# Kernel optimization log

Measured on AMD Instinct MI355X. Metric: run time of the kernel, lower is better.

## Reference

```python
import jax, jax.numpy as jnp
import numpy as np

N_NODES = 100000
N_EDGES = 1600000
N_REL = 8
IN_CH = 64
HIDDEN = 64
OUT_CH = 32


def setup_inputs() -> dict:
    key = jax.random.key(0)
    ks = jax.random.split(key, 10)
    s_in = 1.0 / np.sqrt(IN_CH)
    s_h = 1.0 / np.sqrt(HIDDEN)
    return {
        "x": jax.random.normal(ks[0], (N_NODES, IN_CH), dtype=jnp.float32),
        "edge_index": jax.random.randint(ks[1], (2, N_EDGES), 0, N_NODES, dtype=jnp.int64),
        "edge_type": jax.random.randint(ks[2], (N_EDGES,), 0, N_REL, dtype=jnp.int64),
        "W0": jax.random.normal(ks[3], (N_REL, IN_CH, HIDDEN), dtype=jnp.float32) * s_in,
        "Q0": jax.random.normal(ks[4], (HIDDEN, 1), dtype=jnp.float32) * s_h,
        "K0": jax.random.normal(ks[5], (HIDDEN, 1), dtype=jnp.float32) * s_h,
        "b0": jnp.zeros((HIDDEN,), dtype=jnp.float32),
        "W1": jax.random.normal(ks[6], (N_REL, HIDDEN, OUT_CH), dtype=jnp.float32) * s_h,
        "Q1": jax.random.normal(ks[7], (OUT_CH, 1), dtype=jnp.float32) * (1.0 / np.sqrt(OUT_CH)),
        "K1": jax.random.normal(ks[8], (OUT_CH, 1), dtype=jnp.float32) * (1.0 / np.sqrt(OUT_CH)),
        "b1": jnp.zeros((OUT_CH,), dtype=jnp.float32),
    }


def rgat_conv(x, src, dst, et, W, Q, K, b, n_nodes):
    # relation-typed transform of all nodes: [R, N, out]
    xw = jnp.einsum("ni,rio->rno", x, W)
    # per-node, per-relation attention logits (heads=1, dim=1)
    q = jnp.einsum("rno,od->rnd", xw, Q)[..., 0]  # [R, N]
    k = jnp.einsum("rno,od->rnd", xw, K)[..., 0]  # [R, N]
    # additive self-attention, leaky_relu slope 0.2 (PyG RGATConv default)
    alpha = jax.nn.leaky_relu(q[et, dst] + k[et, src], negative_slope=0.2)  # [E]
    # across-relation segment softmax over incoming edges of each dst node
    amax = jax.ops.segment_max(alpha, dst, num_segments=n_nodes)
    a = jnp.exp(alpha - amax[dst])
    denom = jax.ops.segment_sum(a, dst, num_segments=n_nodes)
    a = a / (denom[dst] + 1e-16)
    # weighted scatter-add aggregation of transformed source features
    msg = a[:, None] * xw[et, src]  # [E, out]
    return jax.ops.segment_sum(msg, dst, num_segments=n_nodes) + b


def reference(x, edge_index, edge_type, W0, Q0, K0, b0, W1, Q1, K1, b1):
    src, dst = edge_index[0], edge_index[1]
    n = x.shape[0]
    h = rgat_conv(x, src, dst, edge_type, W0, Q0, K0, b0, n)
    h = jax.nn.relu(h)  # dropout p=0.0 -> identity
    out = rgat_conv(h, src, dst, edge_type, W1, Q1, K1, b1, n)
    return out
```

## Files before the change

### kernel.cpp

```cpp
#include <hip/hip_runtime.h>
#include <hip/hip_bf16.h>
#include <math.h>


#define CSR_CHUNK 8192

__global__ void k_bhist(const int* __restrict__ dst, int* __restrict__ bcount,
                        int E, int NB) {
    __shared__ int h[512];
    int t = threadIdx.x;
    for (int i = t; i < NB; i += 256) h[i] = 0;
    __syncthreads();
    int e0 = blockIdx.x * CSR_CHUNK;
    int e1 = min(e0 + CSR_CHUNK, E);
    for (int i = e0 + t; i < e1; i += 256) atomicAdd(&h[dst[i] >> 8], 1);
    __syncthreads();
    for (int i = t; i < NB; i += 256) {
        int c = h[i];
        if (c) atomicAdd(&bcount[i], c);
    }
}

__global__ void k_bscan(const int* __restrict__ bcount, int* __restrict__ bstart,
                        int* __restrict__ gcur, int* __restrict__ rowptr,
                        int NB, int N, int E) {
    __shared__ int s[512];
    int t = threadIdx.x;
    int v = (t < NB) ? bcount[t] : 0;
    s[t] = v;
    __syncthreads();
    for (int off = 1; off < 512; off <<= 1) {
        int a = (t >= off) ? s[t - off] : 0;
        __syncthreads();
        s[t] += a;
        __syncthreads();
    }
    int excl = s[t] - v;
    if (t < NB) {
        bstart[t] = excl;
        gcur[t] = excl;
    }
    if (t == 0) {
        bstart[NB] = E;
        rowptr[N] = E;
    }
}

__global__ void k_bscatter(const int* __restrict__ src, const int* __restrict__ dst,
                           const int* __restrict__ et, int* __restrict__ gcur,
                           unsigned* __restrict__ ebuf, int E, int NB) {
    __shared__ int h[512];
    __shared__ int basearr[512];
    int t = threadIdx.x;
    for (int i = t; i < NB; i += 256) h[i] = 0;
    __syncthreads();
    int e0 = blockIdx.x * CSR_CHUNK;
    int e1 = min(e0 + CSR_CHUNK, E);
    for (int i = e0 + t; i < e1; i += 256) atomicAdd(&h[dst[i] >> 8], 1);
    __syncthreads();
    for (int i = t; i < NB; i += 256) {
        int c = h[i];
        basearr[i] = c ? atomicAdd(&gcur[i], c) : 0;
        h[i] = 0;
    }
    __syncthreads();
    for (int i = e0 + t; i < e1; i += 256) {
        int d = dst[i];
        int b = d >> 8;
        int off = atomicAdd(&h[b], 1);
        ebuf[basearr[b] + off] =
            ((unsigned)(d & 255) << 20) | ((unsigned)et[i] << 17) | (unsigned)src[i];
    }
}

__global__ void k_bsort(const unsigned* __restrict__ ebuf, const int* __restrict__ bstart,
                        int* __restrict__ rowptr, int* __restrict__ csr, int N) {
    __shared__ int lh[2048];
    __shared__ int ls[2048];
    __shared__ int ss[256];
    int b = blockIdx.x, t = threadIdx.x;
    int e0 = bstart[b], e1 = bstart[b + 1];
    for (int i = t; i < 2048; i += 256) lh[i] = 0;
    __syncthreads();
    for (int i = e0 + t; i < e1; i += 256) {
        unsigned u = ebuf[i];
        atomicAdd(&lh[(int)(((u >> 20) & 255) * 8 + ((u >> 17) & 7))], 1);
    }
    __syncthreads();
    int loc[8];
    int s = 0;
#pragma unroll
    for (int j = 0; j < 8; j++) {
        loc[j] = s;
        s += lh[t * 8 + j];
    }
    ss[t] = s;
    __syncthreads();
    for (int off = 1; off < 256; off <<= 1) {
        int a = (t >= off) ? ss[t - off] : 0;
        __syncthreads();
        ss[t] += a;
        __syncthreads();
    }
    int excl = ss[t] - s;
#pragma unroll
    for (int j = 0; j < 8; j++) ls[t * 8 + j] = excl + loc[j];
    int node = b * 256 + t;
    if (node < N) rowptr[node] = e0 + excl;
    __syncthreads();
    for (int i = t; i < 2048; i += 256) lh[i] = 0;
    __syncthreads();
    for (int i = e0 + t; i < e1; i += 256) {
        unsigned u = ebuf[i];
        int key = (int)(((u >> 20) & 255) * 8 + ((u >> 17) & 7));
        int off = atomicAdd(&lh[key], 1);
        csr[e0 + ls[key] + off] = (int)(u & 0xFFFFF);
    }
}


__global__ void k_wt2(const float* __restrict__ W, __hip_bfloat16* __restrict__ hi,
                      __hip_bfloat16* __restrict__ lo, int OUT, int total) {
    int t = blockIdx.x * blockDim.x + threadIdx.x;
    if (t < total) {
        int per = 64 * OUT;
        int r = t / per;
        int rem = t % per;
        int i = rem / OUT;
        int o = rem % OUT;
        float v = W[t];
        __hip_bfloat16 h = __float2bfloat16(v);
        __hip_bfloat16 l = __float2bfloat16(v - __bfloat162float(h));
        size_t idx = (size_t)o * 512 + i * 8 + r;
        hi[idx] = h;
        lo[idx] = l;
    }
}

__global__ void k_wqk(const float* W, const float* Qv, const float* Kv,
                      float* wq, float* wk, int OUT) {
    int t = blockIdx.x * blockDim.x + threadIdx.x;
    if (t < 8 * 64) {
        int r = t >> 6, i = t & 63;
        const float* wrow = W + ((size_t)r * 64 + i) * OUT;
        float a = 0.f, b = 0.f;
        for (int o = 0; o < OUT; o++) {
            float w = wrow[o];
            a += w * Qv[o];
            b += w * Kv[o];
        }
        wq[t] = a;
        wk[t] = b;
    }
}

__global__ __launch_bounds__(256) void k_qk2(
        const float* __restrict__ xin, const float* __restrict__ wq,
        const float* __restrict__ wk, float* __restrict__ qn,
        float* __restrict__ kn, unsigned short* __restrict__ xbb, int N) {
    __shared__ float xt[64][65];
    __shared__ float swq[8 * 65], swk[8 * 65];
    int t = threadIdx.x;
    int nb0 = blockIdx.x * 64;
    for (int i = t; i < 512; i += 256) {
        int r = i >> 6, c = i & 63;
        swq[r * 65 + c] = wq[i];
        swk[r * 65 + c] = wk[i];
    }
    for (int i = t; i < 1024; i += 256) {
        int ns = i >> 4;
        int c4 = i & 15;
        int n = nb0 + ns;
        float4 v = {0.f, 0.f, 0.f, 0.f};
        if (n < N) v = ((const float4*)xin)[(size_t)n * 16 + c4];
        xt[ns][c4 * 4 + 0] = v.x;
        xt[ns][c4 * 4 + 1] = v.y;
        xt[ns][c4 * 4 + 2] = v.z;
        xt[ns][c4 * 4 + 3] = v.w;
        if (n < N) {
            __hip_bfloat16 b0 = __float2bfloat16(v.x);
            __hip_bfloat16 b1 = __float2bfloat16(v.y);
            __hip_bfloat16 b2 = __float2bfloat16(v.z);
            __hip_bfloat16 b3 = __float2bfloat16(v.w);
            ushort4 o;
            o.x = *(unsigned short*)&b0;
            o.y = *(unsigned short*)&b1;
            o.z = *(unsigned short*)&b2;
            o.w = *(unsigned short*)&b3;
            *(ushort4*)(xbb + (size_t)n * 64 + c4 * 4) = o;
        }
    }
    __syncthreads();
#pragma unroll
    for (int g = t; g < 512; g += 256) {
        int ns = g >> 3, r = g & 7;
        int n = nb0 + ns;
        if (n < N) {
            float qa = 0.f, ka = 0.f;
#pragma unroll
            for (int i = 0; i < 64; i++) {
                float xv = xt[ns][i];
                qa += xv * swq[r * 65 + i];
                ka += xv * swk[r * 65 + i];
            }
            qn[(size_t)n * 8 + r] = qa;
            kn[(size_t)n * 8 + r] = ka;
        }
    }
}

#define ZSTR 520
#define EMAX 512

#define FLUSH8()                          \
    do {                                  \
        switch (currel) {                 \
            case 0: a0 += racc; break;    \
            case 1: a1 += racc; break;    \
            case 2: a2 += racc; break;    \
            case 3: a3 += racc; break;    \
            case 4: a4 += racc; break;    \
            case 5: a5 += racc; break;    \
            case 6: a6 += racc; break;    \
            case 7: a7 += racc; break;    \
        }                                 \
    } while (0)

template <int OUT, bool RELU>
__global__ __launch_bounds__(256) void k_fused(
        const int* __restrict__ rowptr, const int* __restrict__ csr,
        const float* __restrict__ qn, const float* __restrict__ kn,
        const unsigned short* __restrict__ xb,
        const __hip_bfloat16* __restrict__ wthi,
        const __hip_bfloat16* __restrict__ wtlo,
        const float* __restrict__ bias, float* __restrict__ xout, int N) {
    using v8s = __attribute__((ext_vector_type(8))) short;
    using v4f = __attribute__((ext_vector_type(4))) float;
    __shared__ unsigned short zt[16 * ZSTR];
    __shared__ uint2 s_rec[EMAX];
    __shared__ int s_rp[17];
    __shared__ float s_q[128];
    __shared__ float s_den[16];
    int t = threadIdx.x;
    int wv = t >> 6;
    int lane = t & 63;
    int nb0 = blockIdx.x * 16;

    if (t < 17) {
        int nd = nb0 + t;
        s_rp[t] = rowptr[nd > N ? N : nd];
    }
    if (t < 128) {
        int nd = nb0 + (t >> 3);
        s_q[t] = (nd < N) ? qn[(size_t)nd * 8 + (t & 7)] : 0.f;
    }
    if (t < 16) s_den[t] = 0.f;
    __syncthreads();
    int e0 = s_rp[0];
    int esz = s_rp[16] - e0;

    if (esz <= EMAX) {
        for (int i = t; i < esz; i += 256) {
            int ge = e0 + i;
            int pk = csr[ge];
            int lo = 0;
            lo = (s_rp[lo + 8] <= ge) ? lo + 8 : lo;
            lo = (s_rp[lo + 4] <= ge) ? lo + 4 : lo;
            lo = (s_rp[lo + 2] <= ge) ? lo + 2 : lo;
            lo = (s_rp[lo + 1] <= ge) ? lo + 1 : lo;
            int rel = pk >> 17;
            int src = pk & 0x1FFFF;
            float v = s_q[lo * 8 + rel] + kn[(size_t)src * 8 + rel];
            v = (v >= 0.f) ? v : 0.2f * v;
            float tv = __expf(v);
            atomicAdd(&s_den[lo], tv);
            s_rec[i] = uint2{__float_as_uint(tv), (unsigned)pk};
        }
        __syncthreads();

#pragma unroll 1
        for (int q = 0; q < 4; q++) {
            int nl = wv * 4 + q;
            int r0 = s_rp[nl] - e0;
            int r1 = s_rp[nl + 1] - e0;
            float a0 = 0.f, a1 = 0.f, a2 = 0.f, a3 = 0.f;
            float a4 = 0.f, a5 = 0.f, a6 = 0.f, a7 = 0.f;
            int currel = 0;
            float racc = 0.f;
#pragma unroll 1
            for (int j = r0; j < r1; j += 16) {
                float tvv[16];
                int pkk[16];
#pragma unroll
                for (int u = 0; u < 16; u++) {
                    int ii = j + u;
                    bool ok = ii < r1;
                    ii = ok ? ii : (r1 - 1);
                    uint2 rc = s_rec[ii];
                    tvv[u] = __uint_as_float(
                        __builtin_amdgcn_readfirstlane((int)(ok ? rc.x : 0u)));
                    pkk[u] = __builtin_amdgcn_readfirstlane((int)rc.y);
                }
                unsigned short xu[16];
#pragma unroll
                for (int u = 0; u < 16; u++)
                    xu[u] = xb[(size_t)(pkk[u] & 0x1FFFF) * 64 + lane];
#pragma unroll
                for (int u = 0; u < 16; u++) {
                    int rl = pkk[u] >> 17;
                    if (rl != currel) {
                        FLUSH8();
                        currel = rl;
                        racc = 0.f;
                    }
                    racc += tvv[u] * __uint_as_float(((unsigned)xu[u]) << 16);
                }
            }
            FLUSH8();
            float inv = 1.f / (s_den[nl] + 1e-16f);
            float av[8] = {a0, a1, a2, a3, a4, a5, a6, a7};
            unsigned short us[8];
#pragma unroll
            for (int r = 0; r < 8; r++) {
                __hip_bfloat16 b = __float2bfloat16(av[r] * inv);
                us[r] = *(unsigned short*)&b;
            }
            uint4 pack;
            pack.x = (unsigned)us[0] | ((unsigned)us[1] << 16);
            pack.y = (unsigned)us[2] | ((unsigned)us[3] << 16);
            pack.z = (unsigned)us[4] | ((unsigned)us[5] << 16);
            pack.w = (unsigned)us[6] | ((unsigned)us[7] << 16);
            *(uint4*)&zt[nl * ZSTR + lane * 8] = pack;
        }
    } else {
        for (int q = 0; q < 4; q++) {
            int nl = wv * 4 + q;
            int wid = nb0 + nl;
            uint4 pack = {0u, 0u, 0u, 0u};
            if (wid < N) {
                int r0 = rowptr[wid], r1 = rowptr[wid + 1];
                float qv = (lane < 8) ? qn[wid * 8 + lane] : 0.f;
                float denom = 0.f;
                float a0 = 0.f, a1 = 0.f, a2 = 0.f, a3 = 0.f;
                float a4 = 0.f, a5 = 0.f, a6 = 0.f, a7 = 0.f;
                int currel = 0;
                float racc = 0.f;

                for (int base = r0; base < r1; base += 64) {
                    int s = base + lane;
                    int pk = (s < r1) ? csr[s] : 0;
                    int src = pk & 0x1FFFF;
                    int rel = pk >> 17;
                    float qq = __shfl(qv, rel, 64);
                    float tv = 0.f;
                    if (s < r1) {
                        float v = qq + kn[src * 8 + rel];
                        v = (v >= 0.f) ? v : 0.2f * v;
                        tv = __expf(v);
                    }
                    float ts = tv;
#pragma unroll
                    for (int off = 32; off > 0; off >>= 1) ts += __shfl_xor(ts, off, 64);
                    denom += ts;

                    int cnt = min(64, r1 - base);
                    int tvi = (int)__float_as_uint(tv);
                    for (int j = 0; j < cnt; j += 16) {
                        unsigned p[16];
                        float tf[16];
#pragma unroll
                        for (int u = 0; u < 16; u++) {
                            p[u] = (unsigned)__builtin_amdgcn_readlane(pk, j + u);
                            tf[u] = __uint_as_float(
                                (unsigned)__builtin_amdgcn_readlane(tvi, j + u));
                        }
                        unsigned xg[16];
#pragma unroll
                        for (int u = 0; u < 16; u++)
                            xg[u] = (unsigned)xb[(size_t)(p[u] & 0x1FFFF) * 64 + lane];
#pragma unroll
                        for (int u = 0; u < 16; u++) {
                            int rl = (int)(p[u] >> 17);
                            if (rl != currel) {
                                FLUSH8();
                                currel = rl;
                                racc = 0.f;
                            }
                            racc += tf[u] * __uint_as_float(xg[u] << 16);
                        }
                    }
                }
                FLUSH8();
                float inv = 1.f / (denom + 1e-16f);
                float av[8] = {a0, a1, a2, a3, a4, a5, a6, a7};
                unsigned short us[8];
#pragma unroll
                for (int r = 0; r < 8; r++) {
                    __hip_bfloat16 b = __float2bfloat16(av[r] * inv);
                    us[r] = *(unsigned short*)&b;
                }
                pack.x = (unsigned)us[0] | ((unsigned)us[1] << 16);
                pack.y = (unsigned)us[2] | ((unsigned)us[3] << 16);
                pack.z = (unsigned)us[4] | ((unsigned)us[5] << 16);
                pack.w = (unsigned)us[6] | ((unsigned)us[7] << 16);
            }
            *(uint4*)&zt[nl * ZSTR + lane * 8] = pack;
        }
    }
    __syncthreads();

    int quad = lane >> 4;
    int l15 = lane & 15;
    int nt = wv;
    if (nt * 16 < OUT) {
        const short* wh = (const short*)wthi;
        const short* wl = (const short*)wtlo;
        v4f acc = {0.f, 0.f, 0.f, 0.f};
#pragma unroll
        for (int k0 = 0; k0 < 512; k0 += 32) {
            int koff = k0 + quad * 8;
            v8s A = *(const v8s*)&zt[l15 * ZSTR + koff];
            v8s bh = *(const v8s*)(wh + (size_t)(nt * 16 + l15) * 512 + koff);
            v8s bl = *(const v8s*)(wl + (size_t)(nt * 16 + l15) * 512 + koff);
            acc = __builtin_amdgcn_mfma_f32_16x16x32_bf16(A, bh, acc, 0, 0, 0);
            acc = __builtin_amdgcn_mfma_f32_16x16x32_bf16(A, bl, acc, 0, 0, 0);
        }
        float bcol = bias[nt * 16 + l15];
#pragma unroll
        for (int g = 0; g < 4; g++) {
            int row = nb0 + quad * 4 + g;
            if (row < N) {
                float o = acc[g] + bcol;
                if (RELU) o = fmaxf(o, 0.f);
                xout[(size_t)row * OUT + nt * 16 + l15] = o;
            }
        }
    }
}


extern "C" void kernel_launch(void* const* d_in, const int* in_sizes, int n_in,
                              void* d_out, int out_size, void* d_ws, size_t ws_size,
                              hipStream_t stream) {
    const float* x   = (const float*)d_in[0];
    const int*   ei  = (const int*)d_in[1];
    const int*   et  = (const int*)d_in[2];
    const float* W0  = (const float*)d_in[3];
    const float* Q0  = (const float*)d_in[4];
    const float* K0  = (const float*)d_in[5];
    const float* b0  = (const float*)d_in[6];
    const float* W1  = (const float*)d_in[7];
    const float* Q1  = (const float*)d_in[8];
    const float* K1  = (const float*)d_in[9];
    const float* b1  = (const float*)d_in[10];
    float* out = (float*)d_out;

    const int N = in_sizes[0] / 64;
    const int E = in_sizes[2];
    const int* src = ei;
    const int* dst = ei + E;
    const int NB = (N + 255) >> 8;

    char* p = (char*)d_ws;
    auto alloc = [&](size_t bytes) -> void* {
        void* r = (void*)p;
        p += ((bytes + 255) / 256) * 256;
        return r;
    };
    int* rowptr   = (int*)alloc((size_t)(N + 1) * 4);
    int* bcount   = (int*)alloc(513 * 4);
    int* bstart   = (int*)alloc(513 * 4);
    int* gcur     = (int*)alloc(513 * 4);
    unsigned* ebuf = (unsigned*)alloc((size_t)E * 4);
    int* csr      = (int*)alloc((size_t)E * 4);
    float* wq     = (float*)alloc(8 * 64 * 4);
    float* wk     = (float*)alloc(8 * 64 * 4);
    float* qn     = (float*)alloc((size_t)N * 8 * 4);
    float* kn     = (float*)alloc((size_t)N * 8 * 4);
    __hip_bfloat16* wthi = (__hip_bfloat16*)alloc((size_t)64 * 512 * 2);
    __hip_bfloat16* wtlo = (__hip_bfloat16*)alloc((size_t)64 * 512 * 2);
    float* h      = (float*)alloc((size_t)N * 64 * 4);
    unsigned short* xbb = (unsigned short*)alloc((size_t)N * 64 * 2);

    int nchunks = (E + CSR_CHUNK - 1) / CSR_CHUNK;
    hipMemsetAsync(bcount, 0, (size_t)NB * 4, stream);
    k_bhist<<<nchunks, 256, 0, stream>>>(dst, bcount, E, NB);
    k_bscan<<<1, 512, 0, stream>>>(bcount, bstart, gcur, rowptr, NB, N, E);
    k_bscatter<<<nchunks, 256, 0, stream>>>(src, dst, et, gcur, ebuf, E, NB);
    k_bsort<<<NB, 256, 0, stream>>>(ebuf, bstart, rowptr, csr, N);

    int nfb = (N + 15) / 16;
    int nqkb = (N + 63) / 64;

    k_wqk<<<2, 256, 0, stream>>>(W0, Q0, K0, wq, wk, 64);
    k_qk2<<<nqkb, 256, 0, stream>>>(x, wq, wk, qn, kn, xbb, N);
    k_wt2<<<(8 * 64 * 64 + 255) / 256, 256, 0, stream>>>(W0, wthi, wtlo, 64, 8 * 64 * 64);
    k_fused<64, true><<<nfb, 256, 0, stream>>>(rowptr, csr, qn, kn, xbb,
                                               wthi, wtlo, b0, h, N);

    k_wqk<<<2, 256, 0, stream>>>(W1, Q1, K1, wq, wk, 32);
    k_qk2<<<nqkb, 256, 0, stream>>>(h, wq, wk, qn, kn, xbb, N);
    k_wt2<<<(8 * 64 * 32 + 255) / 256, 256, 0, stream>>>(W1, wthi, wtlo, 32, 8 * 64 * 32);
    k_fused<32, false><<<nfb, 256, 0, stream>>>(rowptr, csr, qn, kn, xbb,
                                                wthi, wtlo, b1, out, N);
}
```

Measured before the change: 438.3 us.

## Double-buffer edge gathers across a wave's four nodes with node id packed in CSR

```diff
diff --git a/kernel.cpp b/kernel.cpp
--- a/kernel.cpp
+++ b/kernel.cpp
@@ -114,7 +114,7 @@
         unsigned u = ebuf[i];
         int key = (int)(((u >> 20) & 255) * 8 + ((u >> 17) & 7));
         int off = atomicAdd(&lh[key], 1);
-        csr[e0 + ls[key] + off] = (int)(u & 0xFFFFF);
+        csr[e0 + ls[key] + off] = (int)u;
     }
 }
 
@@ -226,6 +226,65 @@
         }                                 \
     } while (0)
 
+#define WRITEZ()                                                         \
+    do {                                                                 \
+        if (curnode >= 0) {                                              \
+            float inv = 1.f / (denom + 1e-16f);                          \
+            float av[8] = {a0, a1, a2, a3, a4, a5, a6, a7};              \
+            unsigned short us8[8];                                       \
+            _Pragma("unroll") for (int r = 0; r < 8; r++) {              \
+                __hip_bfloat16 bb = __float2bfloat16(av[r] * inv);       \
+                us8[r] = *(unsigned short*)&bb;                          \
+            }                                                            \
+            uint4 pk4;                                                   \
+            pk4.x = (unsigned)us8[0] | ((unsigned)us8[1] << 16);         \
+            pk4.y = (unsigned)us8[2] | ((unsigned)us8[3] << 16);         \
+            pk4.z = (unsigned)us8[4] | ((unsigned)us8[5] << 16);         \
+            pk4.w = (unsigned)us8[6] | ((unsigned)us8[7] << 16);         \
+            *(uint4*)&zt[curnode * ZSTR + lane * 8] = pk4;               \
+        }                                                                \
+    } while (0)
+
+#define LOADREC(PK, TV, g)                                               \
+    do {                                                                 \
+        int base_ = er0 + (g) * 16;                                      \
+        _Pragma("unroll") for (int u = 0; u < 16; u++) {                 \
+            int ii_ = base_ + u;                                         \
+            bool ok_ = ii_ < er1;                                        \
+            int ic_ = ok_ ? ii_ : (er1 - 1);                             \
+            uint2 rc_ = s_rec[ic_];                                      \
+            TV[u] = __uint_as_float(                                     \
+                __builtin_amdgcn_readfirstlane((int)(ok_ ? rc_.x : 0u)));\
+            PK[u] = __builtin_amdgcn_readfirstlane((int)rc_.y);          \
+        }                                                                \
+    } while (0)
+
+#define ISSUE(PK, XU)                                                    \
+    _Pragma("unroll") for (int u = 0; u < 16; u++)                       \
+        XU[u] = xb[(size_t)(PK[u] & 0x1FFFF) * 64 + lane];
+
+#define DRAIN(PK, TV, XU)                                                \
+    _Pragma("unroll") for (int u = 0; u < 16; u++) {                     \
+        int pk_ = PK[u];                                                 \
+        int nl_ = (pk_ >> 20) & 15;                                      \
+        int rl_ = (pk_ >> 17) & 7;                                       \
+        if (nl_ != curnode) {                                            \
+            FLUSH8();                                                    \
+            WRITEZ();                                                    \
+            curnode = nl_;                                               \
+            currel = rl_;                                                \
+            racc = 0.f;                                                  \
+            denom = 0.f;                                                 \
+            a0 = a1 = a2 = a3 = a4 = a5 = a6 = a7 = 0.f;                 \
+        } else if (rl_ != currel) {                                      \
+            FLUSH8();                                                    \
+            currel = rl_;                                                \
+            racc = 0.f;                                                  \
+        }                                                                \
+        racc += TV[u] * __uint_as_float(((unsigned)XU[u]) << 16);        \
+        denom += TV[u];                                                  \
+    }
+
 template <int OUT, bool RELU>
 __global__ __launch_bounds__(256) void k_fused(
         const int* __restrict__ rowptr, const int* __restrict__ csr,
@@ -240,7 +299,6 @@
     __shared__ uint2 s_rec[EMAX];
     __shared__ int s_rp[17];
     __shared__ float s_q[128];
-    __shared__ float s_den[16];
     int t = threadIdx.x;
     int wv = t >> 6;
     int lane = t & 63;
@@ -254,83 +312,67 @@
         int nd = nb0 + (t >> 3);
         s_q[t] = (nd < N) ? qn[(size_t)nd * 8 + (t & 7)] : 0.f;
     }
-    if (t < 16) s_den[t] = 0.f;
+    {
+        uint4 zz = {0u, 0u, 0u, 0u};
+#pragma unroll
+        for (int q = 0; q < 4; q++)
+            *(uint4*)&zt[(wv * 4 + q) * ZSTR + lane * 8] = zz;
+    }
     __syncthreads();
     int e0 = s_rp[0];
     int esz = s_rp[16] - e0;
 
     if (esz <= EMAX) {
         for (int i = t; i < esz; i += 256) {
-            int ge = e0 + i;
-            int pk = csr[ge];
-            int lo = 0;
-            lo = (s_rp[lo + 8] <= ge) ? lo + 8 : lo;
-            lo = (s_rp[lo + 4] <= ge) ? lo + 4 : lo;
-            lo = (s_rp[lo + 2] <= ge) ? lo + 2 : lo;
-            lo = (s_rp[lo + 1] <= ge) ? lo + 1 : lo;
-            int rel = pk >> 17;
+            int pk = csr[e0 + i];
+            int nl = (pk >> 20) & 15;
+            int rel = (pk >> 17) & 7;
             int src = pk & 0x1FFFF;
-            float v = s_q[lo * 8 + rel] + kn[(size_t)src * 8 + rel];
+            float v = s_q[nl * 8 + rel] + kn[(size_t)src * 8 + rel];
             v = (v >= 0.f) ? v : 0.2f * v;
             float tv = __expf(v);
-            atomicAdd(&s_den[lo], tv);
             s_rec[i] = uint2{__float_as_uint(tv), (unsigned)pk};
         }
         __syncthreads();
 
-#pragma unroll 1
-        for (int q = 0; q < 4; q++) {
-            int nl = wv * 4 + q;
-            int r0 = s_rp[nl] - e0;
-            int r1 = s_rp[nl + 1] - e0;
+        {
+            int er0 = __builtin_amdgcn_readfirstlane(s_rp[wv * 4] - e0);
+            int er1 = __builtin_amdgcn_readfirstlane(s_rp[wv * 4 + 4] - e0);
+            int nG = (er1 - er0 + 15) >> 4;
+            int pkA[16], pkB[16];
+            float tvA[16], tvB[16];
+            unsigned short xuA[16], xuB[16];
             float a0 = 0.f, a1 = 0.f, a2 = 0.f, a3 = 0.f;
             float a4 = 0.f, a5 = 0.f, a6 = 0.f, a7 = 0.f;
-            int currel = 0;
-            float racc = 0.f;
+            float racc = 0.f, denom = 0.f;
+            int currel = 0, curnode = -1;
+
+            if (nG > 0) {
+                LOADREC(pkA, tvA, 0);
+                ISSUE(pkA, xuA);
+                bool curA = true;
 #pragma unroll 1
-            for (int j = r0; j < r1; j += 16) {
-                float tvv[16];
-                int pkk[16];
-#pragma unroll
-                for (int u = 0; u < 16; u++) {
-                    int ii = j + u;
-                    bool ok = ii < r1;
-                    ii = ok ? ii : (r1 - 1);
-                    uint2 rc = s_rec[ii];
-                    tvv[u] = __uint_as_float(
-                        __builtin_amdgcn_readfirstlane((int)(ok ? rc.x : 0u)));
-                    pkk[u] = __builtin_amdgcn_readfirstlane((int)rc.y);
+                for (int g = 0; g < nG; g++) {
+                    if (g + 1 < nG) {
+                        if (curA) {
+                            LOADREC(pkB, tvB, g + 1);
+                            ISSUE(pkB, xuB);
+                        } else {
+                            LOADREC(pkA, tvA, g + 1);
+                            ISSUE(pkA, xuA);
+                        }
+                    }
+                    __builtin_amdgcn_sched_barrier(0);
+                    if (curA) {
+                        DRAIN(pkA, tvA, xuA);
+                    } else {
+                        DRAIN(pkB, tvB, xuB);
+                    }
+                    curA = !curA;
                 }
-                unsigned short xu[16];
-#pragma unroll
-                for (int u = 0; u < 16; u++)
-                    xu[u] = xb[(size_t)(pkk[u] & 0x1FFFF) * 64 + lane];
-#pragma unroll
-                for (int u = 0; u < 16; u++) {
-                    int rl = pkk[u] >> 17;
-                    if (rl != currel) {
-                        FLUSH8();
-                        currel = rl;
-                        racc = 0.f;
-                    }
-                    racc += tvv[u] * __uint_as_float(((unsigned)xu[u]) << 16);
-                }
+                FLUSH8();
+                WRITEZ();
             }
-            FLUSH8();
-            float inv = 1.f / (s_den[nl] + 1e-16f);
-            float av[8] = {a0, a1, a2, a3, a4, a5, a6, a7};
-            unsigned short us[8];
-#pragma unroll
-            for (int r = 0; r < 8; r++) {
-                __hip_bfloat16 b = __float2bfloat16(av[r] * inv);
-                us[r] = *(unsigned short*)&b;
-            }
-            uint4 pack;
-            pack.x = (unsigned)us[0] | ((unsigned)us[1] << 16);
-            pack.y = (unsigned)us[2] | ((unsigned)us[3] << 16);
-            pack.z = (unsigned)us[4] | ((unsigned)us[5] << 16);
-            pack.w = (unsigned)us[6] | ((unsigned)us[7] << 16);
-            *(uint4*)&zt[nl * ZSTR + lane * 8] = pack;
         }
     } else {
         for (int q = 0; q < 4; q++) {
@@ -350,7 +392,7 @@
                     int s = base + lane;
                     int pk = (s < r1) ? csr[s] : 0;
                     int src = pk & 0x1FFFF;
-                    int rel = pk >> 17;
+                    int rel = (pk >> 17) & 7;
                     float qq = __shfl(qv, rel, 64);
                     float tv = 0.f;
                     if (s < r1) {
@@ -380,7 +422,7 @@
                             xg[u] = (unsigned)xb[(size_t)(p[u] & 0x1FFFF) * 64 + lane];
 #pragma unroll
                         for (int u = 0; u < 16; u++) {
-                            int rl = (int)(p[u] >> 17);
+                            int rl = (int)((p[u] >> 17) & 7);
                             if (rl != currel) {
                                 FLUSH8();
                                 currel = rl;
```

Result: slower. 532.6 us (+21.5%).
